# Performance work log

Hardware: AMD Instinct MI355X
Metric: run time of the kernel (lower is better)

Reference implementation:

```python
import jax, jax.numpy as jnp
import numpy as np

B, S, HID = 2, 2048, 1024
NH, NKV, HD = 16, 4, 64
MAXPOS, THETA, EPS = 4096, 10000.0, 1e-6


def _rope_tables():
    inv_freq = 1.0 / (THETA ** (jnp.arange(0, HD, 2, dtype=jnp.float32) / HD))
    t = jnp.arange(MAXPOS, dtype=jnp.float32)
    freqs = jnp.outer(t, inv_freq)                      # [MAXPOS, HD/2]
    emb = jnp.concatenate([freqs, freqs], axis=-1)      # [MAXPOS, HD]
    return jnp.cos(emb), jnp.sin(emb)


def setup_inputs() -> dict:
    key = jax.random.key(0)
    ks = jax.random.split(key, 8)
    cos, sin = _rope_tables()
    neg = jnp.finfo(jnp.float32).min
    causal = jnp.where(jnp.tril(jnp.ones((S, S), dtype=bool)), 0.0, neg)
    sc = 0.02
    return {
        "hidden_states": jax.random.normal(ks[0], (B, S, HID), jnp.float32),
        "cos": cos,
        "sin": sin,
        "position_ids": jnp.broadcast_to(jnp.arange(S, dtype=jnp.int32), (B, S)),
        "attention_mask": causal[None, None, :, :],
        "Wq": jax.random.normal(ks[1], (NH * HD, HID), jnp.float32) * sc,
        "Wk": jax.random.normal(ks[2], (NKV * HD, HID), jnp.float32) * sc,
        "Wv": jax.random.normal(ks[3], (NKV * HD, HID), jnp.float32) * sc,
        "Wo": jax.random.normal(ks[4], (HID, NH * HD), jnp.float32) * sc,
        "q_norm_w": jnp.ones((HD,), jnp.float32),
        "k_norm_w": jnp.ones((HD,), jnp.float32),
    }


def _rms_norm(x, w):
    xf = x.astype(jnp.float32)
    var = jnp.mean(xf * xf, axis=-1, keepdims=True)
    return (w * (xf * jax.lax.rsqrt(var + EPS))).astype(x.dtype)


def _rotate_half(x):
    x1, x2 = jnp.split(x, 2, axis=-1)
    return jnp.concatenate([-x2, x1], axis=-1)


def reference(hidden_states, cos, sin, position_ids, attention_mask,
              Wq, Wk, Wv, Wo, q_norm_w, k_norm_w):
    b, s, _ = hidden_states.shape
    # projections -> [b, heads, s, hd]
    q = (hidden_states @ Wq.T).reshape(b, s, NH, HD).transpose(0, 2, 1, 3)
    k = (hidden_states @ Wk.T).reshape(b, s, NKV, HD).transpose(0, 2, 1, 3)
    v = (hidden_states @ Wv.T).reshape(b, s, NKV, HD).transpose(0, 2, 1, 3)
    # per-head RMS norm on head_dim
    q = _rms_norm(q, q_norm_w)
    k = _rms_norm(k, k_norm_w)
    # rotary embedding (unsqueeze_dim=1 -> broadcast over heads)
    c = cos[position_ids][:, None, :, :]  # [b,1,s,hd]
    sn = sin[position_ids][:, None, :, :]
    q = q * c + _rotate_half(q) * sn
    k = k * c + _rotate_half(k) * sn
    # GQA: repeat kv heads
    n_rep = NH // NKV
    k = jnp.repeat(k, n_rep, axis=1)
    v = jnp.repeat(v, n_rep, axis=1)
    # attention
    scores = jnp.einsum("bhqd,bhkd->bhqk", q, k) / np.sqrt(HD).astype(np.float32)
    scores = scores + attention_mask
    probs = jax.nn.softmax(scores.astype(jnp.float32), axis=-1).astype(q.dtype)
    ctx = jnp.einsum("bhqk,bhkd->bhqd", probs, v)  # [b,NH,s,hd]
    ctx = ctx.transpose(0, 2, 1, 3).reshape(b, s, NH * HD)
    return ctx @ Wo.T
```

## Files before the change

kernel.cpp:

```cpp
#include <hip/hip_runtime.h>
#include <stdint.h>

#define S_LEN 2048
#define HIDDEN 1024
#define NH 16
#define NKV 4
#define HD 64

typedef unsigned short u16;
typedef __attribute__((ext_vector_type(8))) short short8;
typedef __attribute__((ext_vector_type(4))) float f32x4;
typedef __attribute__((ext_vector_type(16))) float f32x16;
typedef __attribute__((ext_vector_type(4))) uint32_t u32x4;

__device__ __forceinline__ u16 f2b(float f) {
  uint32_t u = __float_as_uint(f);
  uint32_t r = u + 0x7fffu + ((u >> 16) & 1u);
  return (u16)(r >> 16);
}
__device__ __forceinline__ float b2f(u16 b) {
  return __uint_as_float(((uint32_t)b) << 16);
}
__device__ __forceinline__ void gll16(const void* g, void* l) {
  __builtin_amdgcn_global_load_lds(
      (const __attribute__((address_space(1))) uint32_t*)g,
      (__attribute__((address_space(3))) uint32_t*)l, 16, 0, 0);
}

__global__ __launch_bounds__(256) void f2b_multi(
    const float* __restrict__ s0, u16* __restrict__ d0, int n0,
    const float* __restrict__ s1, u16* __restrict__ d1, int n1,
    const float* __restrict__ s2, u16* __restrict__ d2, int n2,
    const float* __restrict__ s3, u16* __restrict__ d3, int n3,
    const float* __restrict__ s4, u16* __restrict__ d4, int n4) {
  int i = blockIdx.x * 256 + threadIdx.x;
  const float* s;
  u16* d;
  int idx = i;
  if (i < n0) { s = s0; d = d0; }
  else if ((idx = i - n0) < n1) { s = s1; d = d1; }
  else if ((idx = i - n0 - n1) < n2) { s = s2; d = d2; }
  else if ((idx = i - n0 - n1 - n2) < n3) { s = s3; d = d3; }
  else if ((idx = i - n0 - n1 - n2 - n3) < n4) { s = s4; d = d4; }
  else return;
  f32x4 a = *reinterpret_cast<const f32x4*>(&s[(size_t)idx * 8]);
  f32x4 b = *reinterpret_cast<const f32x4*>(&s[(size_t)idx * 8 + 4]);
  short8 t;
#pragma unroll
  for (int k = 0; k < 4; ++k) t[k] = (short)f2b(a[k]);
#pragma unroll
  for (int k = 0; k < 4; ++k) t[4 + k] = (short)f2b(b[k]);
  *reinterpret_cast<short8*>(&d[(size_t)idx * 8]) = t;
}

template <int OUT_BF16>
__global__ __launch_bounds__(512) void gemm_bt(const u16* __restrict__ A,
                                               const u16* __restrict__ B,
                                               void* __restrict__ Cv,
                                               int M, int N, int K) {
  __shared__ u16 As[128][64];
  __shared__ u16 Bs[128][64];
  const int tid = threadIdx.x;
  const int wid = tid >> 6, lane = tid & 63;
  const int fr = lane & 15, fg = lane >> 4;
  const int m0 = blockIdx.x * 128, n0 = blockIdx.y * 128;
  const int wr = wid >> 2, wc = wid & 3;
  const int srow = lane >> 3, scol = (lane & 7) << 3;
  f32x4 acc[4][2] = {};

  for (int k0 = 0; k0 < K; k0 += 64) {
    __syncthreads();
#pragma unroll
    for (int i = 0; i < 2; ++i) {
      const int c = wid + i * 8;
      gll16(&A[(size_t)(m0 + c * 8 + srow) * K + k0 + scol], &As[c * 8][0]);
      gll16(&B[(size_t)(n0 + c * 8 + srow) * K + k0 + scol], &Bs[c * 8][0]);
    }
    __syncthreads();
#pragma unroll
    for (int ks = 0; ks < 2; ++ks) {
      short8 a[4], b[2];
#pragma unroll
      for (int i = 0; i < 4; ++i)
        a[i] = *reinterpret_cast<const short8*>(
            &As[wr * 64 + i * 16 + fr][ks * 32 + fg * 8]);
#pragma unroll
      for (int j = 0; j < 2; ++j)
        b[j] = *reinterpret_cast<const short8*>(
            &Bs[wc * 32 + j * 16 + fr][ks * 32 + fg * 8]);
#pragma unroll
      for (int i = 0; i < 4; ++i)
#pragma unroll
        for (int j = 0; j < 2; ++j)
          acc[i][j] = __builtin_amdgcn_mfma_f32_16x16x32_bf16(a[i], b[j], acc[i][j], 0, 0, 0);
    }
  }

  const int rb = fg * 4;
#pragma unroll
  for (int i = 0; i < 4; ++i)
#pragma unroll
    for (int j = 0; j < 2; ++j) {
      const int row0 = m0 + wr * 64 + i * 16 + rb;
      const int col = n0 + wc * 32 + j * 16 + fr;
#pragma unroll
      for (int r = 0; r < 4; ++r) {
        size_t idx = (size_t)(row0 + r) * N + col;
        if (OUT_BF16) ((u16*)Cv)[idx] = f2b(acc[i][j][r]);
        else          ((float*)Cv)[idx] = acc[i][j][r];
      }
    }
}

__global__ __launch_bounds__(256) void normrope(const u16* __restrict__ qkv,
                                                const int* __restrict__ pos_ids,
                                                const float* __restrict__ cosT,
                                                const float* __restrict__ sinT,
                                                const float* __restrict__ qw,
                                                const float* __restrict__ kw,
                                                u16* __restrict__ Qn,
                                                u16* __restrict__ Kn) {
  const int w = blockIdx.x * 4 + (threadIdx.x >> 6);
  const int lane = threadIdx.x & 63;
  const int row = w / 20, unit = w % 20;
  const int b = row >> 11, s = row & 2047;
  float x = b2f(qkv[(size_t)row * 1536 + unit * 64 + lane]);
  const bool isq = unit < 16;
  const int h = isq ? unit : unit - 16;
  float ss = x * x;
  ss += __shfl_xor(ss, 1);
  ss += __shfl_xor(ss, 2);
  ss += __shfl_xor(ss, 4);
  ss += __shfl_xor(ss, 8);
  ss += __shfl_xor(ss, 16);
  ss += __shfl_xor(ss, 32);
  float r = rsqrtf(ss * (1.0f / 64.0f) + 1e-6f);
  float xn = x * r * (isq ? qw[lane] * 0.18033688011112042f : kw[lane]);
  const int p = pos_ids[row];
  const float c = cosT[p * 64 + lane];
  const float sn = sinT[p * 64 + lane];
  float partner = __shfl_xor(xn, 32);
  float out = xn * c + (lane < 32 ? -partner : partner) * sn;
  if (isq) Qn[((size_t)(b * NH + h) * S_LEN + s) * HD + lane] = f2b(out);
  else     Kn[((size_t)(b * NKV + h) * S_LEN + s) * HD + lane] = f2b(out);
}

__global__ __launch_bounds__(256) void vtrans(const u16* __restrict__ qkv,
                                              u16* __restrict__ Vt) {
  const int s0 = blockIdx.x * 64;
  const int b = blockIdx.y >> 2, hv = blockIdx.y & 3;
  __shared__ u16 t[64][72];
  const int tid = threadIdx.x;
  const int r = tid >> 2, cq = (tid & 3) << 4;
#pragma unroll
  for (int i = 0; i < 2; ++i)
    *reinterpret_cast<short8*>(&t[r][cq + i * 8]) =
        *reinterpret_cast<const short8*>(
            &qkv[(size_t)(b * S_LEN + s0 + r) * 1536 + 1280 + hv * 64 + cq + i * 8]);
  __syncthreads();
  const int d = tid >> 2, sq = (tid & 3) << 4;
#pragma unroll
  for (int i = 0; i < 2; ++i) {
    u16 tmp[8];
#pragma unroll
    for (int k = 0; k < 8; ++k) tmp[k] = t[sq + i * 8 + k][d];
    *reinterpret_cast<short8*>(
        &Vt[((size_t)(b * NKV + hv) * HD + d) * S_LEN + s0 + sq + i * 8]) =
        *reinterpret_cast<short8*>(tmp);
  }
}

__device__ __forceinline__ void attn_tile(const u16* __restrict__ K,
                                          const u16* __restrict__ V,
                                          const short8 qf[4], int kv0, bool domask,
                                          int col, int hi,
                                          f32x16& o0, f32x16& o1, float& m, float& l) {
  short8 v0 = *reinterpret_cast<const short8*>(&V[(size_t)col * S_LEN + kv0 + hi * 8]);
  short8 v1 = *reinterpret_cast<const short8*>(&V[(size_t)col * S_LEN + kv0 + 16 + hi * 8]);
  short8 v2 = *reinterpret_cast<const short8*>(&V[(size_t)(32 + col) * S_LEN + kv0 + hi * 8]);
  short8 v3 = *reinterpret_cast<const short8*>(&V[(size_t)(32 + col) * S_LEN + kv0 + 16 + hi * 8]);
  f32x16 sA = {}, sB = {};
  {
    short8 k0 = *reinterpret_cast<const short8*>(&K[(size_t)(kv0 + col) * HD + hi * 8]);
    short8 k1 = *reinterpret_cast<const short8*>(&K[(size_t)(kv0 + col) * HD + 16 + hi * 8]);
    short8 k2 = *reinterpret_cast<const short8*>(&K[(size_t)(kv0 + col) * HD + 32 + hi * 8]);
    short8 k3 = *reinterpret_cast<const short8*>(&K[(size_t)(kv0 + col) * HD + 48 + hi * 8]);
    sA = __builtin_amdgcn_mfma_f32_32x32x16_bf16(k0, qf[0], sA, 0, 0, 0);
    sB = __builtin_amdgcn_mfma_f32_32x32x16_bf16(k1, qf[1], sB, 0, 0, 0);
    sA = __builtin_amdgcn_mfma_f32_32x32x16_bf16(k2, qf[2], sA, 0, 0, 0);
    sB = __builtin_amdgcn_mfma_f32_32x32x16_bf16(k3, qf[3], sB, 0, 0, 0);
  }
  f32x16 s = sA + sB;
  if (domask) {
#pragma unroll
    for (int r = 0; r < 16; ++r) {
      int kvr = (r & 3) + 8 * (r >> 2) + 4 * hi;
      s[r] = (kvr <= col) ? s[r] : -3.0e38f;
    }
  }
  float t8[8];
#pragma unroll
  for (int r = 0; r < 8; ++r) t8[r] = fmaxf(s[r], s[r + 8]);
#pragma unroll
  for (int r = 0; r < 4; ++r) t8[r] = fmaxf(t8[r], t8[r + 4]);
  float tm = fmaxf(fmaxf(t8[0], t8[1]), fmaxf(t8[2], t8[3]));
  tm = fmaxf(tm, __shfl_xor(tm, 32));
  if (!__all(tm <= m + 8.0f)) {
    float mn = fmaxf(m, tm);
    float al = exp2f(m - mn);
    m = mn;
    l *= al;
#pragma unroll
    for (int r = 0; r < 16; ++r) { o0[r] *= al; o1[r] *= al; }
  }
  float p[16];
#pragma unroll
  for (int r = 0; r < 16; ++r) p[r] = exp2f(s[r] - m);
  float u8[8];
#pragma unroll
  for (int r = 0; r < 8; ++r) u8[r] = p[r] + p[r + 8];
#pragma unroll
  for (int r = 0; r < 4; ++r) u8[r] += u8[r + 4];
  float ps = (u8[0] + u8[1]) + (u8[2] + u8[3]);
  ps += __shfl_xor(ps, 32);
  l += ps;
  uint32_t w[8], x[8];
#pragma unroll
  for (int i = 0; i < 8; ++i) {
    uint32_t wo;
    asm("v_cvt_pk_bf16_f32 %0, %1, %2" : "=v"(wo) : "v"(p[2 * i]), "v"(p[2 * i + 1]));
    w[i] = wo;
  }
#pragma unroll
  for (int i = 0; i < 8; ++i) x[i] = (uint32_t)__shfl_xor((int)w[i], 32);
  u32x4 bw0 = {hi ? x[2] : w[0], hi ? x[3] : w[1], hi ? w[2] : x[0], hi ? w[3] : x[1]};
  u32x4 bw1 = {hi ? x[6] : w[4], hi ? x[7] : w[5], hi ? w[6] : x[4], hi ? w[7] : x[5]};
  short8 B0 = __builtin_bit_cast(short8, bw0);
  short8 B1 = __builtin_bit_cast(short8, bw1);
  o0 = __builtin_amdgcn_mfma_f32_32x32x16_bf16(v0, B0, o0, 0, 0, 0);
  o0 = __builtin_amdgcn_mfma_f32_32x32x16_bf16(v1, B1, o0, 0, 0, 0);
  o1 = __builtin_amdgcn_mfma_f32_32x32x16_bf16(v2, B0, o1, 0, 0, 0);
  o1 = __builtin_amdgcn_mfma_f32_32x32x16_bf16(v3, B1, o1, 0, 0, 0);
}

__global__ __launch_bounds__(256) void attn_kernel(const u16* __restrict__ Qn,
                                                   const u16* __restrict__ Kn,
                                                   const u16* __restrict__ Vt,
                                                   u16* __restrict__ ctx) {
  const int bh = blockIdx.y;
  const int b = bh >> 4, h = bh & 15, hkv = h >> 2;
  const u16* Q = Qn + (size_t)bh * S_LEN * HD;
  const u16* K = Kn + (size_t)(b * NKV + hkv) * S_LEN * HD;
  const u16* V = Vt + (size_t)(b * NKV + hkv) * HD * S_LEN;
  const int wid = threadIdx.x >> 6, lane = threadIdx.x & 63;
  const int col = lane & 31, hi = lane >> 5;
  const int j = blockIdx.x;
  const int pair = wid >> 1, par = wid & 1;
  const int qt = pair ? j : 63 - j;
  const int q0 = qt * 32;

  __shared__ float Pm[2][32], Pl[2][32];
  __shared__ float Po[2][32][65];
  __shared__ __align__(16) u16 Tl[2][32][72];

  short8 qf[4];
#pragma unroll
  for (int d = 0; d < 4; ++d)
    qf[d] = *reinterpret_cast<const short8*>(&Q[(size_t)(q0 + col) * HD + d * 16 + hi * 8]);

  f32x16 o0 = {}, o1 = {};
  float m = -3.0e38f, l = 0.0f;

  for (int kt = par; kt <= qt; kt += 2)
    attn_tile(K, V, qf, kt * 32, kt == qt, col, hi, o0, o1, m, l);

  if (par) {
    if (hi == 0) { Pm[pair][col] = m; Pl[pair][col] = l; }
#pragma unroll
    for (int r = 0; r < 16; ++r) {
      int dl = (r & 3) + 8 * (r >> 2) + 4 * hi;
      Po[pair][col][dl] = o0[r];
      Po[pair][col][32 + dl] = o1[r];
    }
  }
  __syncthreads();
  if (par) return;

  float m1 = Pm[pair][col], l1 = Pl[pair][col];
  float M = fmaxf(m, m1);
  float w0 = exp2f(m - M), w1 = exp2f(m1 - M);
  float L = w0 * l + w1 * l1;
  const float invL = 1.0f / L;
#pragma unroll
  for (int r = 0; r < 16; ++r) {
    int dl = (r & 3) + 8 * (r >> 2) + 4 * hi;
    float a0 = w0 * o0[r] + w1 * Po[pair][col][dl];
    float a1 = w0 * o1[r] + w1 * Po[pair][col][32 + dl];
    Tl[pair][col][dl] = f2b(a0 * invL);
    Tl[pair][col][32 + dl] = f2b(a1 * invL);
  }
#pragma unroll
  for (int k2 = 0; k2 < 4; ++k2) {
    short8 vv = *reinterpret_cast<const short8*>(&Tl[pair][col][hi * 32 + k2 * 8]);
    *reinterpret_cast<short8*>(
        &ctx[((size_t)(b * S_LEN) + q0 + col) * (NH * HD) + h * HD + hi * 32 + k2 * 8]) = vv;
  }
}

extern "C" void kernel_launch(void* const* d_in, const int* in_sizes, int n_in,
                              void* d_out, int out_size, void* d_ws, size_t ws_size,
                              hipStream_t stream) {
  const float* hidden = (const float*)d_in[0];
  const float* cosT   = (const float*)d_in[1];
  const float* sinT   = (const float*)d_in[2];
  const int*   pos    = (const int*)d_in[3];
  const float* Wq = (const float*)d_in[5];
  const float* Wk = (const float*)d_in[6];
  const float* Wv = (const float*)d_in[7];
  const float* Wo = (const float*)d_in[8];
  const float* qw = (const float*)d_in[9];
  const float* kw = (const float*)d_in[10];

  char* p = (char*)d_ws;
  u16* hb   = (u16*)p; p += (size_t)4096 * 1024 * 2;
  u16* wqkv = (u16*)p; p += (size_t)1536 * 1024 * 2;
  u16* wob  = (u16*)p; p += (size_t)1024 * 1024 * 2;
  u16* qkvr = (u16*)p; p += (size_t)4096 * 1536 * 2;
  u16* qn   = (u16*)p; p += (size_t)(NH * 2) * S_LEN * HD * 2;
  u16* kn   = (u16*)p; p += (size_t)(NKV * 2) * S_LEN * HD * 2;
  u16* vt   = (u16*)p; p += (size_t)(NKV * 2) * HD * S_LEN * 2;
  u16* ctx  = (u16*)p; p += (size_t)4096 * 1024 * 2;

  f2b_multi<<<3332, 256, 0, stream>>>(hidden, hb, 524288,
                                      Wq, wqkv, 131072,
                                      Wk, wqkv + 1048576, 32768,
                                      Wv, wqkv + 1310720, 32768,
                                      Wo, wob, 131072);

  gemm_bt<1><<<dim3(32, 12), 512, 0, stream>>>(hb, wqkv, qkvr, 4096, 1536, 1024);

  normrope<<<20480, 256, 0, stream>>>(qkvr, pos, cosT, sinT, qw, kw, qn, kn);
  vtrans<<<dim3(32, 8), 256, 0, stream>>>(qkvr, vt);

  attn_kernel<<<dim3(32, 2 * NH), 256, 0, stream>>>(qn, kn, vt, ctx);

  gemm_bt<0><<<dim3(32, 8), 512, 0, stream>>>(ctx, wob, d_out, 4096, 1024, 1024);
}
```

Measured before the change: 256.1 us.

## Split attention into KV-chunked partial pass plus merge kernel; permute V to drop shuffles

Replaces the paired-wave attention kernel with a split-KV scheme. Each wave processes a 16-tile KV chunk for one query tile and writes unnormalized bf16 partial outputs plus max and sum to workspace. A separate merge kernel then combines the chunks into ctx. Separately, vtrans now stores V with a permuted sequence order so the P fragment can feed the MFMA directly, which removes the cross-half shuffles. The split aims for better load balance and more parallelism, at the cost of an extra launch, extra global traffic for partials, and bf16 rounding of unnormalized partials.

New measurement: 281.8 us. 1.1x slower.

```diff
diff --git a/kernel.cpp b/kernel.cpp
--- a/kernel.cpp
+++ b/kernel.cpp
@@ -163,7 +163,12 @@
   for (int i = 0; i < 2; ++i) {
     u16 tmp[8];
 #pragma unroll
-    for (int k = 0; k < 8; ++k) tmp[k] = t[sq + i * 8 + k][d];
+    for (int k = 0; k < 8; ++k) {
+      const int sl = sq + i * 8 + k;
+      const int sp = (sl & 32) + 8 * (2 * ((sl >> 4) & 1) + ((sl >> 2) & 1)) +
+                     4 * ((sl >> 3) & 1) + (sl & 3);
+      tmp[k] = t[sp][d];
+    }
     *reinterpret_cast<short8*>(
         &Vt[((size_t)(b * NKV + hv) * HD + d) * S_LEN + s0 + sq + i * 8]) =
         *reinterpret_cast<short8*>(tmp);
@@ -224,17 +229,15 @@
   float ps = (u8[0] + u8[1]) + (u8[2] + u8[3]);
   ps += __shfl_xor(ps, 32);
   l += ps;
-  uint32_t w[8], x[8];
+  uint32_t w[8];
 #pragma unroll
   for (int i = 0; i < 8; ++i) {
     uint32_t wo;
     asm("v_cvt_pk_bf16_f32 %0, %1, %2" : "=v"(wo) : "v"(p[2 * i]), "v"(p[2 * i + 1]));
     w[i] = wo;
   }
-#pragma unroll
-  for (int i = 0; i < 8; ++i) x[i] = (uint32_t)__shfl_xor((int)w[i], 32);
-  u32x4 bw0 = {hi ? x[2] : w[0], hi ? x[3] : w[1], hi ? w[2] : x[0], hi ? w[3] : x[1]};
-  u32x4 bw1 = {hi ? x[6] : w[4], hi ? x[7] : w[5], hi ? w[6] : x[4], hi ? w[7] : x[5]};
+  u32x4 bw0 = {w[0], w[1], w[2], w[3]};
+  u32x4 bw1 = {w[4], w[5], w[6], w[7]};
   short8 B0 = __builtin_bit_cast(short8, bw0);
   short8 B1 = __builtin_bit_cast(short8, bw1);
   o0 = __builtin_amdgcn_mfma_f32_32x32x16_bf16(v0, B0, o0, 0, 0, 0);
@@ -243,25 +246,23 @@
   o1 = __builtin_amdgcn_mfma_f32_32x32x16_bf16(v3, B1, o1, 0, 0, 0);
 }
 
-__global__ __launch_bounds__(256) void attn_kernel(const u16* __restrict__ Qn,
-                                                   const u16* __restrict__ Kn,
-                                                   const u16* __restrict__ Vt,
-                                                   u16* __restrict__ ctx) {
+__global__ __launch_bounds__(256) void attn_pass1(const u16* __restrict__ Qn,
+                                                  const u16* __restrict__ Kn,
+                                                  const u16* __restrict__ Vt,
+                                                  float* __restrict__ PML,
+                                                  u16* __restrict__ PO) {
   const int bh = blockIdx.y;
   const int b = bh >> 4, h = bh & 15, hkv = h >> 2;
+  const int wid = threadIdx.x >> 6, lane = threadIdx.x & 63;
+  const int col = lane & 31, hi = lane >> 5;
+  const int qt = 63 - blockIdx.x;
+  const int ck = wid;
+  if (ck * 16 > qt) return;
+  const int q0 = qt * 32;
   const u16* Q = Qn + (size_t)bh * S_LEN * HD;
   const u16* K = Kn + (size_t)(b * NKV + hkv) * S_LEN * HD;
   const u16* V = Vt + (size_t)(b * NKV + hkv) * HD * S_LEN;
-  const int wid = threadIdx.x >> 6, lane = threadIdx.x & 63;
-  const int col = lane & 31, hi = lane >> 5;
-  const int j = blockIdx.x;
-  const int pair = wid >> 1, par = wid & 1;
-  const int qt = pair ? j : 63 - j;
-  const int q0 = qt * 32;
-
-  __shared__ float Pm[2][32], Pl[2][32];
-  __shared__ float Po[2][32][65];
-  __shared__ __align__(16) u16 Tl[2][32][72];
+  const int slot = (bh * 64 + qt) * 4 + ck;
 
   short8 qf[4];
 #pragma unroll
@@ -270,41 +271,62 @@
 
   f32x16 o0 = {}, o1 = {};
   float m = -3.0e38f, l = 0.0f;
-
-  for (int kt = par; kt <= qt; kt += 2)
+  const int kend = min(ck * 16 + 15, qt);
+  for (int kt = ck * 16; kt <= kend; ++kt)
     attn_tile(K, V, qf, kt * 32, kt == qt, col, hi, o0, o1, m, l);
 
-  if (par) {
-    if (hi == 0) { Pm[pair][col] = m; Pl[pair][col] = l; }
-#pragma unroll
-    for (int r = 0; r < 16; ++r) {
-      int dl = (r & 3) + 8 * (r >> 2) + 4 * hi;
-      Po[pair][col][dl] = o0[r];
-      Po[pair][col][32 + dl] = o1[r];
-    }
-  }
-  __syncthreads();
-  if (par) return;
-
-  float m1 = Pm[pair][col], l1 = Pl[pair][col];
-  float M = fmaxf(m, m1);
-  float w0 = exp2f(m - M), w1 = exp2f(m1 - M);
-  float L = w0 * l + w1 * l1;
-  const float invL = 1.0f / L;
+  __shared__ __align__(16) u16 Tl[4][32][72];
 #pragma unroll
   for (int r = 0; r < 16; ++r) {
     int dl = (r & 3) + 8 * (r >> 2) + 4 * hi;
-    float a0 = w0 * o0[r] + w1 * Po[pair][col][dl];
-    float a1 = w0 * o1[r] + w1 * Po[pair][col][32 + dl];
-    Tl[pair][col][dl] = f2b(a0 * invL);
-    Tl[pair][col][32 + dl] = f2b(a1 * invL);
+    Tl[wid][col][dl] = f2b(o0[r]);
+    Tl[wid][col][32 + dl] = f2b(o1[r]);
   }
 #pragma unroll
   for (int k2 = 0; k2 < 4; ++k2) {
-    short8 vv = *reinterpret_cast<const short8*>(&Tl[pair][col][hi * 32 + k2 * 8]);
+    short8 vv = *reinterpret_cast<const short8*>(&Tl[wid][col][hi * 32 + k2 * 8]);
     *reinterpret_cast<short8*>(
-        &ctx[((size_t)(b * S_LEN) + q0 + col) * (NH * HD) + h * HD + hi * 32 + k2 * 8]) = vv;
-  }
+        &PO[(size_t)slot * 2048 + col * 64 + hi * 32 + k2 * 8]) = vv;
+  }
+  if (hi == 0) {
+    PML[slot * 64 + col] = m;
+    PML[slot * 64 + 32 + col] = l;
+  }
+}
+
+__global__ __launch_bounds__(256) void attn_merge(const float* __restrict__ PML,
+                                                  const u16* __restrict__ PO,
+                                                  u16* __restrict__ ctx) {
+  const int qt = blockIdx.x, bh = blockIdx.y;
+  const int b = bh >> 4, h = bh & 15;
+  const int t = threadIdx.x;
+  const int q = t >> 3, d0 = (t & 7) * 8;
+  const int nck = (qt >> 4) + 1;
+  const int base = (bh * 64 + qt) * 4;
+
+  float M = -3.0e38f;
+#pragma unroll 4
+  for (int ck = 0; ck < nck; ++ck)
+    M = fmaxf(M, PML[(base + ck) * 64 + q]);
+  float L = 0.0f;
+  float acc[8] = {};
+#pragma unroll 4
+  for (int ck = 0; ck < nck; ++ck) {
+    float mm = PML[(base + ck) * 64 + q];
+    float ll = PML[(base + ck) * 64 + 32 + q];
+    float w = exp2f(mm - M);
+    L += w * ll;
+    short8 ov = *reinterpret_cast<const short8*>(
+        &PO[(size_t)(base + ck) * 2048 + q * 64 + d0]);
+#pragma unroll
+    for (int k = 0; k < 8; ++k) acc[k] += w * b2f((u16)ov[k]);
+  }
+  const float invL = 1.0f / L;
+  short8 outv;
+#pragma unroll
+  for (int k = 0; k < 8; ++k) outv[k] = (short)f2b(acc[k] * invL);
+  *reinterpret_cast<short8*>(
+      &ctx[((size_t)(b * S_LEN) + qt * 32 + q) * (NH * HD) + h * HD + d0]) = outv;
 }
 
 extern "C" void kernel_launch(void* const* d_in, const int* in_sizes, int n_in,
@@ -330,6 +352,8 @@
   u16* kn   = (u16*)p; p += (size_t)(NKV * 2) * S_LEN * HD * 2;
   u16* vt   = (u16*)p; p += (size_t)(NKV * 2) * HD * S_LEN * 2;
   u16* ctx  = (u16*)p; p += (size_t)4096 * 1024 * 2;
+  float* pml = (float*)p; p += (size_t)8192 * 64 * 4;
+  u16* po   = (u16*)p; p += (size_t)8192 * 2048 * 2;
 
   f2b_multi<<<3332, 256, 0, stream>>>(hidden, hb, 524288,
                                       Wq, wqkv, 131072,
@@ -342,7 +366,8 @@
   normrope<<<20480, 256, 0, stream>>>(qkvr, pos, cosT, sinT, qw, kw, qn, kn);
   vtrans<<<dim3(32, 8), 256, 0, stream>>>(qkvr, vt);
 
-  attn_kernel<<<dim3(32, 2 * NH), 256, 0, stream>>>(qn, kn, vt, ctx);
+  attn_pass1<<<dim3(64, 2 * NH), 256, 0, stream>>>(qn, kn, vt, pml, po);
+  attn_merge<<<dim3(64, 2 * NH), 256, 0, stream>>>(pml, po, ctx);
 
   gemm_bt<0><<<dim3(32, 8), 512, 0, stream>>>(ctx, wob, d_out, 4096, 1024, 1024);
 }
```
